# Kernel optimization log

Hardware: AMD Instinct MI355X
Metric: run time of the kernel (lower is better)

The kernel has to match this reference:

```python
import jax, jax.numpy as jnp
import numpy as np
from jax import lax

B, HIST, FC, N, F = 64, 24, 24, 1000, 8
EMB, HID, NEMB, OUT = 32, 64, 1000, 1
IN = EMB + OUT  # GRU input dim


def setup_inputs() -> dict:
    key = jax.random.key(0)
    ks = jax.random.split(key, 11)
    X = jax.random.normal(ks[0], (B, HIST + FC, N, F), jnp.float32)
    idx = jax.random.randint(ks[1], (B, HIST + FC, N), 0, NEMB)
    X = X.at[..., -1].set(idx.astype(jnp.float32))  # last channel = spatial ids
    hn = jax.random.normal(ks[2], (B * N, HID), jnp.float32)
    xn = jax.random.normal(ks[3], (B, N, OUT), jnp.float32)
    s = 0.1
    emb_table = jax.random.normal(ks[4], (NEMB, EMB), jnp.float32) * s
    W_ih = jax.random.normal(ks[5], (3 * HID, IN), jnp.float32) * s
    W_hh = jax.random.normal(ks[6], (3 * HID, HID), jnp.float32) * s
    b_ih = jax.random.normal(ks[7], (3 * HID,), jnp.float32) * s
    b_hh = jax.random.normal(ks[8], (3 * HID,), jnp.float32) * s
    W_out = jax.random.normal(ks[9], (OUT, HID), jnp.float32) * s
    b_out = jax.random.normal(ks[10], (OUT,), jnp.float32) * s
    return {"X": X, "hn": hn, "xn": xn, "emb_table": emb_table,
            "W_ih": W_ih, "W_hh": W_hh, "b_ih": b_ih, "b_hh": b_hh,
            "W_out": W_out, "b_out": b_out}


def reference(X, hn, xn, emb_table, W_ih, W_hh, b_ih, b_hh, W_out, b_out):
    # indices for the forecast steps: [FC, B, N]
    idx_seq = X[:, :FC, :, -1].astype(jnp.int32).transpose(1, 0, 2)

    def step(carry, idx_t):
        h, x_prev = carry                      # h: [B*N, HID], x_prev: [B, N, 1]
        emb = emb_table[idx_t]                 # [B, N, EMB] gather
        x = jnp.concatenate([x_prev, emb], axis=-1).reshape(B * N, IN)
        gi = x @ W_ih.T + b_ih                 # [B*N, 3*HID]
        gh = h @ W_hh.T + b_hh
        i_r, i_z, i_n = jnp.split(gi, 3, axis=-1)
        h_r, h_z, h_n = jnp.split(gh, 3, axis=-1)
        r = jax.nn.sigmoid(i_r + h_r)
        z = jax.nn.sigmoid(i_z + h_z)
        n = jnp.tanh(i_n + r * h_n)
        h_new = (1.0 - z) * n + z * h
        out = h_new.reshape(B, N, HID) @ W_out.T + b_out  # [B, N, 1]
        return (h_new, out), out

    _, preds = lax.scan(step, (hn, xn), idx_seq)  # preds: [FC, B, N, 1]
    return preds.transpose(1, 0, 2, 3)            # [B, FC, N, 1]
```

## Files before the change

### kernel.cpp

```cpp
#include <hip/hip_runtime.h>
#include <math.h>

#define BB   64
#define FC   24
#define NN   1000
#define HID  64
#define EMBD 32
#define TT   48
#define FF   8
#define INSZ 33

#define CPB  16
#define TPB  256
#define AST  72
#define XST  40

#define NL2E (-1.4426950408889634f)
#define TL2E ( 2.8853900817779268f)

typedef __attribute__((ext_vector_type(8))) short bf16x8;
typedef __attribute__((ext_vector_type(4))) float f32x4;

static __device__ __forceinline__ unsigned short f2bf(float f) {
    unsigned u = __builtin_bit_cast(unsigned, f);
    u += 0x7FFFu + ((u >> 16) & 1u);
    return (unsigned short)(u >> 16);
}
static __device__ __forceinline__ unsigned cvt_pk_bf16(float a, float b) {
    unsigned r;
    asm("v_cvt_pk_bf16_f32 %0, %1, %2" : "=v"(r) : "v"(a), "v"(b));
    return r;
}
static __device__ __forceinline__ bf16x8 mk_bf8(float4 lo, float4 hi, float s) {
    union { unsigned u[4]; bf16x8 v; } r;
    r.u[0] = cvt_pk_bf16(lo.x * s, lo.y * s);
    r.u[1] = cvt_pk_bf16(lo.z * s, lo.w * s);
    r.u[2] = cvt_pk_bf16(hi.x * s, hi.y * s);
    r.u[3] = cvt_pk_bf16(hi.z * s, hi.w * s);
    return r.v;
}

static __device__ __forceinline__ void lds_barrier() {
    __builtin_amdgcn_sched_barrier(0);
    asm volatile("s_waitcnt lgkmcnt(0)" ::: "memory");
    __builtin_amdgcn_s_barrier();
    __builtin_amdgcn_sched_barrier(0);
}

__global__ __launch_bounds__(TPB) __attribute__((amdgpu_waves_per_eu(4)))
void gru_decoder(
    const float* __restrict__ X,
    const float* __restrict__ hn0,
    const float* __restrict__ xn,
    const float* __restrict__ emb,
    const float* __restrict__ Wih,
    const float* __restrict__ Whh,
    const float* __restrict__ bih,
    const float* __restrict__ bhh,
    const float* __restrict__ Wout,
    const float* __restrict__ bout,
    float* __restrict__ out)
{
    __shared__ __align__(16) unsigned short Hbuf[2][CPB * AST];
    __shared__ __align__(16) unsigned short Xt[2][CPB * XST];
    __shared__ int   idxbuf[FC * CPB];
    __shared__ float xbuf0[CPB];

    const int tid  = threadIdx.x;
    const int lane = tid & 63;
    const int g    = tid >> 6;
    const int quad = lane >> 4;
    const int l15  = lane & 15;
    const int jcol = g * 16 + l15;
    const int rowb = quad * 4;
    const int cell0 = blockIdx.x * CPB;

    for (int e = tid; e < FC * CPB; e += TPB) {
        int t = e >> 4, m = e & 15;
        int cell = cell0 + m;
        int b = cell / NN, n = cell - b * NN;
        idxbuf[t * CPB + m] = (int)X[(((size_t)b * TT + t) * NN + n) * FF + 7];
    }
    if (tid < CPB) xbuf0[tid] = xn[cell0 + tid];

    bf16x8 Bf[3][2];
    #pragma unroll
    for (int gate = 0; gate < 3; ++gate) {
        const float s = (gate < 2) ? NL2E : TL2E;
        #pragma unroll
        for (int ks = 0; ks < 2; ++ks) {
            const float* src = Whh + (size_t)(gate * HID + jcol) * HID + ks * 32 + quad * 8;
            Bf[gate][ks] = mk_bf8(*(const float4*)src, *(const float4*)(src + 4), s);
        }
    }
    bf16x8 BX[3];
    #pragma unroll
    for (int gate = 0; gate < 3; ++gate) {
        const float s = (gate < 2) ? NL2E : TL2E;
        const float* src = Wih + (size_t)(gate * HID + jcol) * INSZ + 1 + quad * 8;
        union { unsigned u[4]; bf16x8 v; } f;
        #pragma unroll
        for (int p = 0; p < 4; ++p)
            f.u[p] = cvt_pk_bf16(src[2 * p] * s, src[2 * p + 1] * s);
        BX[gate] = f.v;
    }
    bf16x8 BO[2];
    #pragma unroll
    for (int ks = 0; ks < 2; ++ks) {
        const float* src = Wout + ks * 32 + quad * 8;
        union { unsigned u[4]; bf16x8 v; } f;
        #pragma unroll
        for (int p = 0; p < 4; ++p)
            f.u[p] = cvt_pk_bf16(src[2 * p], src[2 * p + 1]);
        BO[ks] = f.v;
    }

    const float w0r2 = NL2E * Wih[(size_t)jcol * INSZ];
    const float w0z2 = NL2E * Wih[(size_t)(HID + jcol) * INSZ];
    const float w0n2 = TL2E * Wih[(size_t)(2 * HID + jcol) * INSZ];
    const float bout0 = bout[0];
    const float br2p  = NL2E * (bih[jcol] + bhh[jcol]) + w0r2 * bout0;
    const float bz2p  = NL2E * (bih[HID + jcol] + bhh[HID + jcol]) + w0z2 * bout0;
    const float bni2p = TL2E * bih[2 * HID + jcol] + w0n2 * bout0;
    const float bhn2  = TL2E * bhh[2 * HID + jcol];

    size_t sb[4];
    #pragma unroll
    for (int rr = 0; rr < 4; ++rr) {
        int cell = cell0 + rowb + rr;
        int b = cell / NN, n = cell - b * NN;
        sb[rr] = (size_t)b * FC * NN + n;
    }
    const bool storer = (g == 0) && (l15 == 0);

    float hold[4];
    #pragma unroll
    for (int rr = 0; rr < 4; ++rr) {
        int m = rowb + rr;
        float h = hn0[((size_t)cell0 + m) * HID + jcol];
        hold[rr] = h;
        Hbuf[0][m * AST + jcol] = f2bf(h);
    }
    __syncthreads();

    const int r8 = tid >> 3, k4 = (tid & 7) * 4;
    const bool stg = tid < CPB * 8;
    if (stg) {
        int idx = idxbuf[r8];
        float4 e4 = *(const float4*)(emb + (size_t)idx * EMBD + k4);
        *(uint2*)&Xt[0][r8 * XST + k4] =
            make_uint2(cvt_pk_bf16(e4.x, e4.y), cvt_pk_bf16(e4.z, e4.w));
    }
    __syncthreads();

    f32x4 ar, az, ani, ang, ao;

    auto PHASE_A = [&](const unsigned short* Hb, const unsigned short* Xc) {
        const bf16x8 a0 = *(const bf16x8*)&Hb[l15 * AST + quad * 8];
        const bf16x8 a1 = *(const bf16x8*)&Hb[l15 * AST + 32 + quad * 8];
        const bf16x8 x0 = *(const bf16x8*)&Xc[l15 * XST + quad * 8];
        const f32x4 z4 = {0.f, 0.f, 0.f, 0.f};
        ar  = __builtin_amdgcn_mfma_f32_16x16x32_bf16(x0, BX[0], z4, 0, 0, 0);
        ar  = __builtin_amdgcn_mfma_f32_16x16x32_bf16(a0, Bf[0][0], ar, 0, 0, 0);
        ar  = __builtin_amdgcn_mfma_f32_16x16x32_bf16(a1, Bf[0][1], ar, 0, 0, 0);
        az  = __builtin_amdgcn_mfma_f32_16x16x32_bf16(x0, BX[1], z4, 0, 0, 0);
        az  = __builtin_amdgcn_mfma_f32_16x16x32_bf16(a0, Bf[1][0], az, 0, 0, 0);
        az  = __builtin_amdgcn_mfma_f32_16x16x32_bf16(a1, Bf[1][1], az, 0, 0, 0);
        ani = __builtin_amdgcn_mfma_f32_16x16x32_bf16(x0, BX[2], z4, 0, 0, 0);
        ang = __builtin_amdgcn_mfma_f32_16x16x32_bf16(a0, Bf[2][0], z4, 0, 0, 0);
        ang = __builtin_amdgcn_mfma_f32_16x16x32_bf16(a1, Bf[2][1], ang, 0, 0, 0);
        ao  = __builtin_amdgcn_mfma_f32_16x16x32_bf16(a0, BO[0], z4, 0, 0, 0);
        ao  = __builtin_amdgcn_mfma_f32_16x16x32_bf16(a1, BO[1], ao, 0, 0, 0);
    };

    auto GATES = [&](int rr, float xv) -> float {
        float sr = fmaf(w0r2, xv, ar[rr] + br2p);
        float r  = __builtin_amdgcn_rcpf(1.0f + __builtin_amdgcn_exp2f(sr));
        float sz = fmaf(w0z2, xv, az[rr] + bz2p);
        float z  = __builtin_amdgcn_rcpf(1.0f + __builtin_amdgcn_exp2f(sz));
        float v  = fmaf(r, ang[rr] + bhn2, fmaf(w0n2, xv, ani[rr] + bni2p));
        float e  = __builtin_amdgcn_exp2f(v);
        float nv = fmaf(-2.0f, __builtin_amdgcn_rcpf(e + 1.0f), 1.0f);
        float hnew = fmaf(z, hold[rr] - nv, nv);
        hold[rr] = hnew;
        return hnew;
    };

    auto WRITE_H = [&](unsigned short* Hw, int rp, float h0, float h1) {
        unsigned pk = cvt_pk_bf16(h0, h1);
        const int m0 = rowb + rp * 2;
        Hw[m0 * AST + jcol]       = (unsigned short)pk;
        Hw[(m0 + 1) * AST + jcol] = (unsigned short)(pk >> 16);
    };

    {
        float4 e4 = {0.f, 0.f, 0.f, 0.f};
        if (stg) {
            int idx = idxbuf[1 * CPB + r8];
            e4 = *(const float4*)(emb + (size_t)idx * EMBD + k4);
        }
        PHASE_A(Hbuf[0], Xt[0]);
        #pragma unroll
        for (int rp = 0; rp < 2; ++rp) {
            float h0 = GATES(rp * 2,     xbuf0[rowb + rp * 2]     - bout0);
            float h1 = GATES(rp * 2 + 1, xbuf0[rowb + rp * 2 + 1] - bout0);
            WRITE_H(Hbuf[1], rp, h0, h1);
        }
        if (stg)
            *(uint2*)&Xt[1][r8 * XST + k4] =
                make_uint2(cvt_pk_bf16(e4.x, e4.y), cvt_pk_bf16(e4.z, e4.w));
        lds_barrier();
    }

    #pragma unroll 2
    for (int t = 1; t < FC; ++t) {
        const int tn = (t + 1 < FC) ? t + 1 : FC - 1;
        float4 e4 = {0.f, 0.f, 0.f, 0.f};
        if (stg)
            e4 = *(const float4*)(emb + (size_t)idxbuf[tn * CPB + r8] * EMBD + k4);

        PHASE_A(Hbuf[t & 1], Xt[t & 1]);

        unsigned short* Hw = Hbuf[(t + 1) & 1];
        #pragma unroll
        for (int rp = 0; rp < 2; ++rp) {
            float h0 = GATES(rp * 2,     ao[rp * 2]);
            float h1 = GATES(rp * 2 + 1, ao[rp * 2 + 1]);
            WRITE_H(Hw, rp, h0, h1);
        }
        if (storer) {
            #pragma unroll
            for (int rr = 0; rr < 4; ++rr)
                out[sb[rr] + (size_t)(t - 1) * NN] = ao[rr] + bout0;
        }
        if (stg)
            *(uint2*)&Xt[(t + 1) & 1][r8 * XST + k4] =
                make_uint2(cvt_pk_bf16(e4.x, e4.y), cvt_pk_bf16(e4.z, e4.w));
        lds_barrier();
    }

    {
        const unsigned short* Hb = Hbuf[FC & 1];
        const bf16x8 a0 = *(const bf16x8*)&Hb[l15 * AST + quad * 8];
        const bf16x8 a1 = *(const bf16x8*)&Hb[l15 * AST + 32 + quad * 8];
        const f32x4 z4 = {0.f, 0.f, 0.f, 0.f};
        f32x4 o = __builtin_amdgcn_mfma_f32_16x16x32_bf16(a0, BO[0], z4, 0, 0, 0);
        o = __builtin_amdgcn_mfma_f32_16x16x32_bf16(a1, BO[1], o, 0, 0, 0);
        if (storer) {
            #pragma unroll
            for (int rr = 0; rr < 4; ++rr)
                out[sb[rr] + (size_t)(FC - 1) * NN] = o[rr] + bout0;
        }
    }
}

extern "C" void kernel_launch(void* const* d_in, const int* in_sizes, int n_in,
                              void* d_out, int out_size, void* d_ws, size_t ws_size,
                              hipStream_t stream) {
    (void)in_sizes; (void)n_in; (void)out_size; (void)d_ws; (void)ws_size;
    const float* X    = (const float*)d_in[0];
    const float* hn   = (const float*)d_in[1];
    const float* xn   = (const float*)d_in[2];
    const float* emb  = (const float*)d_in[3];
    const float* Wih  = (const float*)d_in[4];
    const float* Whh  = (const float*)d_in[5];
    const float* bih  = (const float*)d_in[6];
    const float* bhh  = (const float*)d_in[7];
    const float* Wout = (const float*)d_in[8];
    const float* bout = (const float*)d_in[9];
    float* out = (float*)d_out;

    const int blocks = (BB * NN) / CPB;
    gru_decoder<<<blocks, TPB, 0, stream>>>(X, hn, xn, emb, Wih, Whh,
                                            bih, bhh, Wout, bout, out);
}
```

Baseline: 268.8 us.

## Run each 16-cell tile in a single wave and drop block barriers

Shrinks each block from four waves to one wave, which now computes all 64 hidden columns of a 16-cell tile. Per-step workgroup barriers become compiler-only fences, and the h buffer is single-buffered in LDS. The recurrent input term x_prev*W_ih[:,0] is folded into the W_hh weights through W_out, which removes the per-step dependency on the output projection. In exchange, each wave holds many more weight fragments in registers (waves_per_eu lowered to 2), and correctness relies on wave-level LDS ordering without explicit waitcnt.

```diff
diff --git a/kernel.cpp b/kernel.cpp
--- a/kernel.cpp
+++ b/kernel.cpp
@@ -10,8 +10,7 @@
 #define FF   8
 #define INSZ 33
 
-#define CPB  16
-#define TPB  256
+#define CPW  16
 #define AST  72
 #define XST  40
 
@@ -21,11 +20,6 @@
 typedef __attribute__((ext_vector_type(8))) short bf16x8;
 typedef __attribute__((ext_vector_type(4))) float f32x4;
 
-static __device__ __forceinline__ unsigned short f2bf(float f) {
-    unsigned u = __builtin_bit_cast(unsigned, f);
-    u += 0x7FFFu + ((u >> 16) & 1u);
-    return (unsigned short)(u >> 16);
-}
 static __device__ __forceinline__ unsigned cvt_pk_bf16(float a, float b) {
     unsigned r;
     asm("v_cvt_pk_bf16_f32 %0, %1, %2" : "=v"(r) : "v"(a), "v"(b));
@@ -40,14 +34,12 @@
     return r.v;
 }
 
-static __device__ __forceinline__ void lds_barrier() {
+static __device__ __forceinline__ void wave_fence() {
+    asm volatile("" ::: "memory");
     __builtin_amdgcn_sched_barrier(0);
-    asm volatile("s_waitcnt lgkmcnt(0)" ::: "memory");
-    __builtin_amdgcn_s_barrier();
-    __builtin_amdgcn_sched_barrier(0);
-}
-
-__global__ __launch_bounds__(TPB) __attribute__((amdgpu_waves_per_eu(4)))
+}
+
+__global__ __launch_bounds__(64) __attribute__((amdgpu_waves_per_eu(2)))
 void gru_decoder(
     const float* __restrict__ X,
     const float* __restrict__ hn0,
@@ -61,50 +53,71 @@
     const float* __restrict__ bout,
     float* __restrict__ out)
 {
-    __shared__ __align__(16) unsigned short Hbuf[2][CPB * AST];
-    __shared__ __align__(16) unsigned short Xt[2][CPB * XST];
-    __shared__ int   idxbuf[FC * CPB];
-    __shared__ float xbuf0[CPB];
-
-    const int tid  = threadIdx.x;
-    const int lane = tid & 63;
-    const int g    = tid >> 6;
+    __shared__ __align__(16) unsigned short Hbuf[CPW * AST];
+    __shared__ __align__(16) unsigned short Xt[2][CPW * XST];
+    __shared__ int idxbuf[(FC + 1) * CPW];
+
+    const int lane = threadIdx.x;
     const int quad = lane >> 4;
     const int l15  = lane & 15;
-    const int jcol = g * 16 + l15;
-    const int rowb = quad * 4;
-    const int cell0 = blockIdx.x * CPB;
-
-    for (int e = tid; e < FC * CPB; e += TPB) {
+    const int cell0 = blockIdx.x * CPW;
+
+    for (int e = lane; e < (FC + 1) * CPW; e += 64) {
         int t = e >> 4, m = e & 15;
+        int tt = (t < FC) ? t : FC - 1;
         int cell = cell0 + m;
         int b = cell / NN, n = cell - b * NN;
-        idxbuf[t * CPB + m] = (int)X[(((size_t)b * TT + t) * NN + n) * FF + 7];
-    }
-    if (tid < CPB) xbuf0[tid] = xn[cell0 + tid];
-
-    bf16x8 Bf[3][2];
+        idxbuf[e] = (int)X[(((size_t)b * TT + tt) * NN + n) * FF + 7];
+    }
+    wave_fence();
+
+    const float bout0 = bout[0];
+
+    float br4[4], bz4[4], bni4[4], bhn4[4], w0n24[4], w0r24[4], w0z24[4];
+    #pragma unroll
+    for (int cg = 0; cg < 4; ++cg) {
+        const int hid = l15 * 4 + cg;
+        w0r24[cg] = NL2E * Wih[(size_t)hid * INSZ];
+        w0z24[cg] = NL2E * Wih[(size_t)(HID + hid) * INSZ];
+        w0n24[cg] = TL2E * Wih[(size_t)(2 * HID + hid) * INSZ];
+        br4[cg]  = NL2E * (bih[hid] + bhh[hid]) + w0r24[cg] * bout0;
+        bz4[cg]  = NL2E * (bih[HID + hid] + bhh[HID + hid]) + w0z24[cg] * bout0;
+        bni4[cg] = TL2E * bih[2 * HID + hid] + w0n24[cg] * bout0;
+        bhn4[cg] = TL2E * bhh[2 * HID + hid];
+    }
+
+    bf16x8 Bf[3][4][2];
+    bf16x8 BX[3][4];
+    bf16x8 BO[2];
     #pragma unroll
     for (int gate = 0; gate < 3; ++gate) {
         const float s = (gate < 2) ? NL2E : TL2E;
         #pragma unroll
-        for (int ks = 0; ks < 2; ++ks) {
-            const float* src = Whh + (size_t)(gate * HID + jcol) * HID + ks * 32 + quad * 8;
-            Bf[gate][ks] = mk_bf8(*(const float4*)src, *(const float4*)(src + 4), s);
-        }
-    }
-    bf16x8 BX[3];
-    #pragma unroll
-    for (int gate = 0; gate < 3; ++gate) {
-        const float s = (gate < 2) ? NL2E : TL2E;
-        const float* src = Wih + (size_t)(gate * HID + jcol) * INSZ + 1 + quad * 8;
-        union { unsigned u[4]; bf16x8 v; } f;
-        #pragma unroll
-        for (int p = 0; p < 4; ++p)
-            f.u[p] = cvt_pk_bf16(src[2 * p] * s, src[2 * p + 1] * s);
-        BX[gate] = f.v;
-    }
-    bf16x8 BO[2];
+        for (int cg = 0; cg < 4; ++cg) {
+            const int hid = l15 * 4 + cg;
+            const float wf = (gate == 0) ? Wih[(size_t)hid * INSZ]
+                          : (gate == 1) ? Wih[(size_t)(HID + hid) * INSZ] : 0.0f;
+            const float* wr = Whh + (size_t)(gate * HID + hid) * HID;
+            #pragma unroll
+            for (int ks = 0; ks < 2; ++ks) {
+                float4 lo = *(const float4*)(wr + ks * 32 + quad * 8);
+                float4 hi = *(const float4*)(wr + ks * 32 + quad * 8 + 4);
+                float4 wl = *(const float4*)(Wout + ks * 32 + quad * 8);
+                float4 wh = *(const float4*)(Wout + ks * 32 + quad * 8 + 4);
+                lo.x = fmaf(wf, wl.x, lo.x); lo.y = fmaf(wf, wl.y, lo.y);
+                lo.z = fmaf(wf, wl.z, lo.z); lo.w = fmaf(wf, wl.w, lo.w);
+                hi.x = fmaf(wf, wh.x, hi.x); hi.y = fmaf(wf, wh.y, hi.y);
+                hi.z = fmaf(wf, wh.z, hi.z); hi.w = fmaf(wf, wh.w, hi.w);
+                Bf[gate][cg][ks] = mk_bf8(lo, hi, s);
+            }
+            const float* wx = Wih + (size_t)(gate * HID + hid) * INSZ + 1 + quad * 8;
+            union { unsigned u[4]; bf16x8 v; } f;
+            #pragma unroll
+            for (int p = 0; p < 4; ++p)
+                f.u[p] = cvt_pk_bf16(wx[2 * p] * s, wx[2 * p + 1] * s);
+            BX[gate][cg] = f.v;
+        }
+    }
     #pragma unroll
     for (int ks = 0; ks < 2; ++ks) {
         const float* src = Wout + ks * 32 + quad * 8;
@@ -115,135 +128,117 @@
         BO[ks] = f.v;
     }
 
-    const float w0r2 = NL2E * Wih[(size_t)jcol * INSZ];
-    const float w0z2 = NL2E * Wih[(size_t)(HID + jcol) * INSZ];
-    const float w0n2 = TL2E * Wih[(size_t)(2 * HID + jcol) * INSZ];
-    const float bout0 = bout[0];
-    const float br2p  = NL2E * (bih[jcol] + bhh[jcol]) + w0r2 * bout0;
-    const float bz2p  = NL2E * (bih[HID + jcol] + bhh[HID + jcol]) + w0z2 * bout0;
-    const float bni2p = TL2E * bih[2 * HID + jcol] + w0n2 * bout0;
-    const float bhn2  = TL2E * bhh[2 * HID + jcol];
-
     size_t sb[4];
     #pragma unroll
     for (int rr = 0; rr < 4; ++rr) {
-        int cell = cell0 + rowb + rr;
+        int cell = cell0 + quad * 4 + rr;
         int b = cell / NN, n = cell - b * NN;
         sb[rr] = (size_t)b * FC * NN + n;
     }
-    const bool storer = (g == 0) && (l15 == 0);
-
-    float hold[4];
-    #pragma unroll
-    for (int rr = 0; rr < 4; ++rr) {
-        int m = rowb + rr;
-        float h = hn0[((size_t)cell0 + m) * HID + jcol];
-        hold[rr] = h;
-        Hbuf[0][m * AST + jcol] = f2bf(h);
-    }
-    __syncthreads();
-
-    const int r8 = tid >> 3, k4 = (tid & 7) * 4;
-    const bool stg = tid < CPB * 8;
-    if (stg) {
-        int idx = idxbuf[r8];
-        float4 e4 = *(const float4*)(emb + (size_t)idx * EMBD + k4);
-        *(uint2*)&Xt[0][r8 * XST + k4] =
-            make_uint2(cvt_pk_bf16(e4.x, e4.y), cvt_pk_bf16(e4.z, e4.w));
-    }
-    __syncthreads();
-
-    f32x4 ar, az, ani, ang, ao;
-
-    auto PHASE_A = [&](const unsigned short* Hb, const unsigned short* Xc) {
-        const bf16x8 a0 = *(const bf16x8*)&Hb[l15 * AST + quad * 8];
-        const bf16x8 a1 = *(const bf16x8*)&Hb[l15 * AST + 32 + quad * 8];
+    const bool storer = (l15 == 0);
+
+    float hold[16];
+    float x0v[4];
+    #pragma unroll
+    for (int reg = 0; reg < 4; ++reg) {
+        float4 h4 = *(const float4*)(hn0 + ((size_t)cell0 + quad * 4 + reg) * HID + l15 * 4);
+        hold[0 + reg] = h4.x; hold[4 + reg] = h4.y;
+        hold[8 + reg] = h4.z; hold[12 + reg] = h4.w;
+        *(uint2*)&Hbuf[(quad * 4 + reg) * AST + l15 * 4] =
+            make_uint2(cvt_pk_bf16(h4.x, h4.y), cvt_pk_bf16(h4.z, h4.w));
+        x0v[reg] = xn[cell0 + quad * 4 + reg];
+    }
+
+    const int r4 = lane >> 2, kq = (lane & 3) * 8;
+    {
+        int idx = idxbuf[r4];
+        float4 ea = *(const float4*)(emb + (size_t)idx * EMBD + kq);
+        float4 eb = *(const float4*)(emb + (size_t)idx * EMBD + kq + 4);
+        union { unsigned u[4]; bf16x8 v; } f;
+        f.u[0] = cvt_pk_bf16(ea.x, ea.y); f.u[1] = cvt_pk_bf16(ea.z, ea.w);
+        f.u[2] = cvt_pk_bf16(eb.x, eb.y); f.u[3] = cvt_pk_bf16(eb.z, eb.w);
+        *(bf16x8*)&Xt[0][r4 * XST + kq] = f.v;
+    }
+
+    const f32x4 z4 = {0.f, 0.f, 0.f, 0.f};
+    f32x4 ao;
+
+    auto STEP = [&](const unsigned short* Xc, bool peel) {
+        wave_fence();
+        const bf16x8 a0 = *(const bf16x8*)&Hbuf[l15 * AST + quad * 8];
+        const bf16x8 a1 = *(const bf16x8*)&Hbuf[l15 * AST + 32 + quad * 8];
         const bf16x8 x0 = *(const bf16x8*)&Xc[l15 * XST + quad * 8];
-        const f32x4 z4 = {0.f, 0.f, 0.f, 0.f};
-        ar  = __builtin_amdgcn_mfma_f32_16x16x32_bf16(x0, BX[0], z4, 0, 0, 0);
-        ar  = __builtin_amdgcn_mfma_f32_16x16x32_bf16(a0, Bf[0][0], ar, 0, 0, 0);
-        ar  = __builtin_amdgcn_mfma_f32_16x16x32_bf16(a1, Bf[0][1], ar, 0, 0, 0);
-        az  = __builtin_amdgcn_mfma_f32_16x16x32_bf16(x0, BX[1], z4, 0, 0, 0);
-        az  = __builtin_amdgcn_mfma_f32_16x16x32_bf16(a0, Bf[1][0], az, 0, 0, 0);
-        az  = __builtin_amdgcn_mfma_f32_16x16x32_bf16(a1, Bf[1][1], az, 0, 0, 0);
-        ani = __builtin_amdgcn_mfma_f32_16x16x32_bf16(x0, BX[2], z4, 0, 0, 0);
-        ang = __builtin_amdgcn_mfma_f32_16x16x32_bf16(a0, Bf[2][0], z4, 0, 0, 0);
-        ang = __builtin_amdgcn_mfma_f32_16x16x32_bf16(a1, Bf[2][1], ang, 0, 0, 0);
-        ao  = __builtin_amdgcn_mfma_f32_16x16x32_bf16(a0, BO[0], z4, 0, 0, 0);
-        ao  = __builtin_amdgcn_mfma_f32_16x16x32_bf16(a1, BO[1], ao, 0, 0, 0);
+        ao = __builtin_amdgcn_mfma_f32_16x16x32_bf16(a0, BO[0], z4, 0, 0, 0);
+        ao = __builtin_amdgcn_mfma_f32_16x16x32_bf16(a1, BO[1], ao, 0, 0, 0);
+        #pragma unroll
+        for (int cg = 0; cg < 4; ++cg) {
+            f32x4 ar = __builtin_amdgcn_mfma_f32_16x16x32_bf16(x0, BX[0][cg], z4, 0, 0, 0);
+            ar = __builtin_amdgcn_mfma_f32_16x16x32_bf16(a0, Bf[0][cg][0], ar, 0, 0, 0);
+            ar = __builtin_amdgcn_mfma_f32_16x16x32_bf16(a1, Bf[0][cg][1], ar, 0, 0, 0);
+            f32x4 az = __builtin_amdgcn_mfma_f32_16x16x32_bf16(x0, BX[1][cg], z4, 0, 0, 0);
+            az = __builtin_amdgcn_mfma_f32_16x16x32_bf16(a0, Bf[1][cg][0], az, 0, 0, 0);
+            az = __builtin_amdgcn_mfma_f32_16x16x32_bf16(a1, Bf[1][cg][1], az, 0, 0, 0);
+            f32x4 ani = __builtin_amdgcn_mfma_f32_16x16x32_bf16(x0, BX[2][cg], z4, 0, 0, 0);
+            f32x4 ang = __builtin_amdgcn_mfma_f32_16x16x32_bf16(a0, Bf[2][cg][0], z4, 0, 0, 0);
+            ang = __builtin_amdgcn_mfma_f32_16x16x32_bf16(a1, Bf[2][cg][1], ang, 0, 0, 0);
+            #pragma unroll
+            for (int reg = 0; reg < 4; ++reg) {
+                float arv = ar[reg] + br4[cg];
+                float azv = az[reg] + bz4[cg];
+                float xnv = ao[reg];
+                if (peel) {
+                    float xc = x0v[reg] - bout0 - ao[reg];
+                    arv = fmaf(w0r24[cg], xc, arv);
+                    azv = fmaf(w0z24[cg], xc, azv);
+                    xnv = x0v[reg] - bout0;
+                }
+                float r = __builtin_amdgcn_rcpf(1.0f + __builtin_amdgcn_exp2f(arv));
+                float z = __builtin_amdgcn_rcpf(1.0f + __builtin_amdgcn_exp2f(azv));
+                float v = fmaf(r, ang[reg] + bhn4[cg],
+                               fmaf(w0n24[cg], xnv, ani[reg] + bni4[cg]));
+                float e = __builtin_amdgcn_exp2f(v);
+                float nv = fmaf(-2.0f, __builtin_amdgcn_rcpf(e + 1.0f), 1.0f);
+                hold[cg * 4 + reg] = fmaf(z, hold[cg * 4 + reg] - nv, nv);
+            }
+        }
+        wave_fence();
+        #pragma unroll
+        for (int reg = 0; reg < 4; ++reg)
+            *(uint2*)&Hbuf[(quad * 4 + reg) * AST + l15 * 4] =
+                make_uint2(cvt_pk_bf16(hold[reg], hold[4 + reg]),
+                           cvt_pk_bf16(hold[8 + reg], hold[12 + reg]));
     };
 
-    auto GATES = [&](int rr, float xv) -> float {
-        float sr = fmaf(w0r2, xv, ar[rr] + br2p);
-        float r  = __builtin_amdgcn_rcpf(1.0f + __builtin_amdgcn_exp2f(sr));
-        float sz = fmaf(w0z2, xv, az[rr] + bz2p);
-        float z  = __builtin_amdgcn_rcpf(1.0f + __builtin_amdgcn_exp2f(sz));
-        float v  = fmaf(r, ang[rr] + bhn2, fmaf(w0n2, xv, ani[rr] + bni2p));
-        float e  = __builtin_amdgcn_exp2f(v);
-        float nv = fmaf(-2.0f, __builtin_amdgcn_rcpf(e + 1.0f), 1.0f);
-        float hnew = fmaf(z, hold[rr] - nv, nv);
-        hold[rr] = hnew;
-        return hnew;
+    auto STAGE_X = [&](int tt, unsigned short* dst) {
+        int idx = idxbuf[tt * CPW + r4];
+        float4 ea = *(const float4*)(emb + (size_t)idx * EMBD + kq);
+        float4 eb = *(const float4*)(emb + (size_t)idx * EMBD + kq + 4);
+        union { unsigned u[4]; bf16x8 v; } f;
+        f.u[0] = cvt_pk_bf16(ea.x, ea.y); f.u[1] = cvt_pk_bf16(ea.z, ea.w);
+        f.u[2] = cvt_pk_bf16(eb.x, eb.y); f.u[3] = cvt_pk_bf16(eb.z, eb.w);
+        *(bf16x8*)&dst[r4 * XST + kq] = f.v;
     };
 
-    auto WRITE_H = [&](unsigned short* Hw, int rp, float h0, float h1) {
-        unsigned pk = cvt_pk_bf16(h0, h1);
-        const int m0 = rowb + rp * 2;
-        Hw[m0 * AST + jcol]       = (unsigned short)pk;
-        Hw[(m0 + 1) * AST + jcol] = (unsigned short)(pk >> 16);
-    };
-
-    {
-        float4 e4 = {0.f, 0.f, 0.f, 0.f};
-        if (stg) {
-            int idx = idxbuf[1 * CPB + r8];
-            e4 = *(const float4*)(emb + (size_t)idx * EMBD + k4);
-        }
-        PHASE_A(Hbuf[0], Xt[0]);
-        #pragma unroll
-        for (int rp = 0; rp < 2; ++rp) {
-            float h0 = GATES(rp * 2,     xbuf0[rowb + rp * 2]     - bout0);
-            float h1 = GATES(rp * 2 + 1, xbuf0[rowb + rp * 2 + 1] - bout0);
-            WRITE_H(Hbuf[1], rp, h0, h1);
-        }
-        if (stg)
-            *(uint2*)&Xt[1][r8 * XST + k4] =
-                make_uint2(cvt_pk_bf16(e4.x, e4.y), cvt_pk_bf16(e4.z, e4.w));
-        lds_barrier();
-    }
-
-    #pragma unroll 2
+    STEP(Xt[0], true);
+    STAGE_X(1, Xt[1]);
+
+    unsigned short* xcur = Xt[1];
+    unsigned short* xnxt = Xt[0];
     for (int t = 1; t < FC; ++t) {
-        const int tn = (t + 1 < FC) ? t + 1 : FC - 1;
-        float4 e4 = {0.f, 0.f, 0.f, 0.f};
-        if (stg)
-            e4 = *(const float4*)(emb + (size_t)idxbuf[tn * CPB + r8] * EMBD + k4);
-
-        PHASE_A(Hbuf[t & 1], Xt[t & 1]);
-
-        unsigned short* Hw = Hbuf[(t + 1) & 1];
-        #pragma unroll
-        for (int rp = 0; rp < 2; ++rp) {
-            float h0 = GATES(rp * 2,     ao[rp * 2]);
-            float h1 = GATES(rp * 2 + 1, ao[rp * 2 + 1]);
-            WRITE_H(Hw, rp, h0, h1);
-        }
+        STEP(xcur, false);
         if (storer) {
             #pragma unroll
             for (int rr = 0; rr < 4; ++rr)
                 out[sb[rr] + (size_t)(t - 1) * NN] = ao[rr] + bout0;
         }
-        if (stg)
-            *(uint2*)&Xt[(t + 1) & 1][r8 * XST + k4] =
-                make_uint2(cvt_pk_bf16(e4.x, e4.y), cvt_pk_bf16(e4.z, e4.w));
-        lds_barrier();
+        STAGE_X(t + 1, xnxt);
+        unsigned short* tmp = xcur; xcur = xnxt; xnxt = tmp;
     }
 
     {
-        const unsigned short* Hb = Hbuf[FC & 1];
-        const bf16x8 a0 = *(const bf16x8*)&Hb[l15 * AST + quad * 8];
-        const bf16x8 a1 = *(const bf16x8*)&Hb[l15 * AST + 32 + quad * 8];
-        const f32x4 z4 = {0.f, 0.f, 0.f, 0.f};
+        wave_fence();
+        const bf16x8 a0 = *(const bf16x8*)&Hbuf[l15 * AST + quad * 8];
+        const bf16x8 a1 = *(const bf16x8*)&Hbuf[l15 * AST + 32 + quad * 8];
         f32x4 o = __builtin_amdgcn_mfma_f32_16x16x32_bf16(a0, BO[0], z4, 0, 0, 0);
         o = __builtin_amdgcn_mfma_f32_16x16x32_bf16(a1, BO[1], o, 0, 0, 0);
         if (storer) {
@@ -270,7 +265,7 @@
     const float* bout = (const float*)d_in[9];
     float* out = (float*)d_out;
 
-    const int blocks = (BB * NN) / CPB;
-    gru_decoder<<<blocks, TPB, 0, stream>>>(X, hn, xn, emb, Wih, Whh,
-                                            bih, bhh, Wout, bout, out);
-}
+    const int blocks = (BB * NN) / CPW;
+    gru_decoder<<<blocks, 64, 0, stream>>>(X, hn, xn, emb, Wih, Whh,
+                                           bih, bhh, Wout, bout, out);
+}
```

After: 282.2 us. +5.0%, slower.
